# Kernel optimization log

Hardware: AMD Instinct MI355X
Metric: run time of the kernel (lower is better)

## Reference

```python
import jax, jax.numpy as jnp
import numpy as np

B, L, D = 32, 512, 128
H, D0, D2 = 8, 32, 32
SIGMA = 1.0
NEG = -10000.0


def setup_inputs() -> dict:
    key = jax.random.key(0)
    k_x, k_m, k1, k2, k3, k_w = jax.random.split(key, 6)
    X = jax.random.normal(k_x, (B, L, D), dtype=jnp.float32)
    # random padding mask; guarantee at least one valid item per row
    mask = jax.random.uniform(k_m, (B, L)) < 0.9
    mask = mask.at[:, 0].set(True)
    # nn.Linear(d, H*d0, bias=False): weight shape [H*d0, d], y = x @ W^T
    W1 = SIGMA * jax.random.normal(k1, (H * D0, D), dtype=jnp.float32)
    W2 = SIGMA * jax.random.normal(k2, (H * D0, D), dtype=jnp.float32)
    W3 = SIGMA * jax.random.normal(k3, (H * D2, D), dtype=jnp.float32)
    w = SIGMA * jax.random.normal(k_w, (H, D2), dtype=jnp.float32)
    return {"X": X, "mask": mask, "W1": W1, "W2": W2, "W3": W3, "w": w}


def reference(X, mask, W1, W2, W3, w):
    b, l, d = X.shape
    h, d2 = w.shape
    d0 = W1.shape[0] // h
    Q = (X @ W1.T).reshape(b, l, h, d0)
    K = (X @ W2.T).reshape(b, l, h, d0)
    V = (X @ W3.T).reshape(b, l, h, d2)
    # scores: [B, H, L, L]
    scores = jnp.einsum('blhd,bmhd->bhlm', Q, K) / jnp.sqrt(jnp.asarray(d0, X.dtype))
    # outer-product symmetric pad mask [B,1,L,L]
    am = (mask[:, None, None, :] & mask[:, None, :, None])
    scores = jnp.where(am, scores, jnp.asarray(NEG, X.dtype))
    attn = jax.nn.softmax(scores, axis=-1)
    out = jnp.einsum('bhlm,bmhd->blhd', attn, V)  # [B,L,H,D2]
    v = jnp.einsum('blhd,hd->bl', out, w) / jnp.sqrt(jnp.asarray(h, X.dtype))
    v = jnp.where(mask, v, jnp.asarray(NEG, X.dtype))
    probs = jax.nn.softmax(v, axis=-1)
    return probs
```

## Files before the change

kernel.cpp:

```cpp
#include <hip/hip_runtime.h>
#include <hip/hip_bf16.h>


typedef __attribute__((ext_vector_type(8))) short bf16x8;
typedef __attribute__((ext_vector_type(4))) float f32x4;
typedef __attribute__((ext_vector_type(8))) unsigned short ushort8;
typedef __attribute__((ext_vector_type(4))) unsigned short ushort4v;

#define NEG (-10000.0f)
#define LOG2E 1.4426950408889634f
#define QSCALE (0.17677669529663687f * LOG2E)

__device__ __forceinline__ unsigned short bf16_rn(float x, float* rep) {
  unsigned u = __float_as_uint(x);
  unsigned r = (u + 0x7FFFu + ((u >> 16) & 1u)) >> 16;
  *rep = __uint_as_float(r << 16);
  return (unsigned short)r;
}

__global__ __launch_bounds__(256) void convert_kernel(
    const float* __restrict__ X, const float* __restrict__ W1,
    const float* __restrict__ W2, const float* __restrict__ W3,
    const float* __restrict__ w,
    unsigned short* __restrict__ X2, unsigned short* __restrict__ Wc) {
  const int bx = blockIdx.x, t = threadIdx.x;
  if (bx < 1056) {
    const float* src;
    unsigned short* dst;
    int row, c;
    if (bx < 1024) {
      const size_t flat = (size_t)bx * 2048 + t * 8;
      row = (int)(flat >> 7); c = (int)(flat & 127);
      src = &X[flat];
      dst = &X2[(size_t)row * 256 + c];
    } else {
      const int flat = (bx - 1024) * 2048 + t * 8;
      row = flat >> 7; c = flat & 127;
      src = (row < 256) ? &W1[(size_t)row * 128 + c]
                        : &W2[(size_t)(row - 256) * 128 + c];
      dst = &Wc[(size_t)row * 256 + c];
    }
    float xv[8];
    *(float4*)&xv[0] = *(const float4*)src;
    *(float4*)&xv[4] = *(const float4*)(src + 4);
    ushort8 hi, lo;
#pragma unroll
    for (int i = 0; i < 8; ++i) {
      float hf, lf;
      hi[i] = bf16_rn(xv[i], &hf);
      lo[i] = bf16_rn(xv[i] - hf, &lf);
    }
    *(ushort8*)dst = hi;
    *(ushort8*)(dst + 128) = lo;
  } else {
    __shared__ float uS[8][128];
    if (t < 128) {
#pragma unroll
      for (int h = 0; h < 8; ++h) {
        float acc = 0.f;
#pragma unroll
        for (int d = 0; d < 32; ++d)
          acc += W3[(h * 32 + d) * 128 + t] * w[h * 32 + d];
        uS[h][t] = acc * 0.3535533905932738f;
      }
    }
    __syncthreads();
    {
      const int r = t >> 5, c = (t & 31) * 4;
      float4 v = *(float4*)&uS[r][c];
      float vv[4] = {v.x, v.y, v.z, v.w};
      ushort4v hi, lo;
#pragma unroll
      for (int i = 0; i < 4; ++i) {
        float hf, lf;
        hi[i] = bf16_rn(vv[i], &hf);
        lo[i] = bf16_rn(vv[i] - hf, &lf);
      }
      *(ushort4v*)&Wc[(size_t)(512 + r) * 256 + c] = hi;
      *(ushort4v*)&Wc[(size_t)(512 + r) * 256 + 128 + c] = lo;
    }
    const ushort8 z = {};
    for (int i = t; i < 1792; i += 256)
      *(ushort8*)&Wc[(size_t)520 * 256 + i * 8] = z;
  }
}

__global__ __launch_bounds__(256) void proj_kernel(
    const unsigned short* __restrict__ X2, const unsigned short* __restrict__ Wc,
    unsigned short* __restrict__ Q2, unsigned short* __restrict__ K2,
    float* __restrict__ Vw) {
  __shared__ unsigned short XS[128][72], WSd[64][72], WSx[64][72];
  const int t = threadIdx.x;
  const int row0 = blockIdx.x * 128, col0 = blockIdx.y * 64;
  const int w = t >> 6, lane = t & 63, g = lane >> 4, r16 = lane & 15;

  f32x4 acc[2][4];
#pragma unroll
  for (int mm = 0; mm < 2; ++mm)
#pragma unroll
    for (int n = 0; n < 4; ++n) acc[mm][n] = (f32x4){0.f, 0.f, 0.f, 0.f};

  for (int kc = 0; kc < 256; kc += 64) {
    const int kcx = (kc + 128) & 255;
    if (kc) __syncthreads();
    {
#pragma unroll
      for (int i = 0; i < 4; ++i) {
        const int flat = i * 256 + t, row = flat >> 3, cg = (flat & 7) * 8;
        *(ushort8*)&XS[row][cg] =
            *(const ushort8*)&X2[(size_t)(row0 + row) * 256 + kc + cg];
      }
#pragma unroll
      for (int i = 0; i < 2; ++i) {
        const int flat = i * 256 + t, row = flat >> 3, cg = (flat & 7) * 8;
        const size_t wb = (size_t)(col0 + row) * 256;
        *(ushort8*)&WSd[row][cg] = *(const ushort8*)&Wc[wb + kc + cg];
        *(ushort8*)&WSx[row][cg] = *(const ushort8*)&Wc[wb + kcx + cg];
      }
    }
    __syncthreads();
#pragma unroll
    for (int ks = 0; ks < 2; ++ks) {
      bf16x8 ah[2];
#pragma unroll
      for (int mm = 0; mm < 2; ++mm)
        ah[mm] = *(const bf16x8*)&XS[w * 32 + mm * 16 + r16][ks * 32 + g * 8];
#pragma unroll
      for (int n = 0; n < 4; ++n) {
        bf16x8 bd = *(const bf16x8*)&WSd[n * 16 + r16][ks * 32 + g * 8];
        bf16x8 bx = *(const bf16x8*)&WSx[n * 16 + r16][ks * 32 + g * 8];
#pragma unroll
        for (int mm = 0; mm < 2; ++mm) {
          acc[mm][n] = __builtin_amdgcn_mfma_f32_16x16x32_bf16(ah[mm], bd, acc[mm][n], 0, 0, 0);
          acc[mm][n] = __builtin_amdgcn_mfma_f32_16x16x32_bf16(ah[mm], bx, acc[mm][n], 0, 0, 0);
        }
      }
    }
  }
#pragma unroll
  for (int n = 0; n < 4; ++n) {
    const int col = col0 + n * 16 + r16;
#pragma unroll
    for (int mm = 0; mm < 2; ++mm) {
#pragma unroll
      for (int r = 0; r < 4; ++r) {
        const int row = row0 + w * 32 + mm * 16 + g * 4 + r;
        const int b = row >> 9, l = row & 511;
        const float val = acc[mm][n][r];
        if (col < 256) {
          const float sv = val * QSCALE;
          float hf, lf;
          const unsigned short hb = bf16_rn(sv, &hf);
          const unsigned short lb = bf16_rn(sv - hf, &lf);
          const size_t o = ((size_t)(b * 8 + (col >> 5)) * 512 + l) * 64 + (col & 31);
          Q2[o] = hb; Q2[o + 32] = lb;
        } else if (col < 512) {
          const int c2 = col - 256;
          float hf, lf;
          const unsigned short hb = bf16_rn(val, &hf);
          const unsigned short lb = bf16_rn(val - hf, &lf);
          const size_t o = ((size_t)(b * 8 + (c2 >> 5)) * 512 + l) * 64 + (c2 & 31);
          K2[o] = hb; K2[o + 32] = lb;
        } else if (col < 520) {
          Vw[(size_t)(b * 8 + (col - 512)) * 512 + l] = val;
        }
      }
    }
  }
}

__global__ __launch_bounds__(512, 4) void attn_kernel(
    const unsigned short* __restrict__ Q2, const unsigned short* __restrict__ K2,
    const float* __restrict__ Vw, const int* __restrict__ mask,
    float* __restrict__ vws) {
  __shared__ unsigned short KS[512][72];
  __shared__ float VwS[512], biasS[512];
  const int t = threadIdx.x;
  const int w = t >> 6, lane = t & 63, g = lane >> 4, r16 = lane & 15;
  const int qbase = blockIdx.x * 256, h = blockIdx.y, b = blockIdx.z;
  const size_t headoff = (size_t)(b * 8 + h) * 512;

#pragma unroll
  for (int i = 0; i < 8; ++i) {
    const int flat = i * 512 + t;
    const int row = flat >> 3, cg = (flat & 7) * 8;
    *(ushort8*)&KS[row][cg] = *(const ushort8*)&K2[(headoff + row) * 64 + cg];
  }
  VwS[t] = Vw[headoff + t];
  biasS[t] = mask[b * 512 + t] ? 0.f : NEG * LOG2E;

  bf16x8 qf[2][2];
#pragma unroll
  for (int qt = 0; qt < 2; ++qt)
#pragma unroll
    for (int ks = 0; ks < 2; ++ks)
      qf[qt][ks] = *(const bf16x8*)
          &Q2[(headoff + qbase + w * 32 + qt * 16 + r16) * 64 + ks * 32 + g * 8];

  __syncthreads();

  float m[2] = {-1e30f, -1e30f}, lsum[2] = {0.f, 0.f}, val[2] = {0.f, 0.f};

  for (int c = 0; c < 8; ++c) {
    bf16x8 a0[4], a1[4];
#pragma unroll
    for (int j = 0; j < 4; ++j) {
      a0[j] = *(const bf16x8*)&KS[c * 64 + j * 16 + r16][g * 8];
      a1[j] = *(const bf16x8*)&KS[c * 64 + j * 16 + r16][32 + g * 8];
    }
    f32x4 sc[4][2];
#pragma unroll
    for (int j = 0; j < 4; ++j)
#pragma unroll
      for (int qt = 0; qt < 2; ++qt) {
        f32x4 z = (f32x4){0.f, 0.f, 0.f, 0.f};
        z = __builtin_amdgcn_mfma_f32_16x16x32_bf16(a0[j], qf[qt][0], z, 0, 0, 0);
        z = __builtin_amdgcn_mfma_f32_16x16x32_bf16(a0[j], qf[qt][1], z, 0, 0, 0);
        z = __builtin_amdgcn_mfma_f32_16x16x32_bf16(a1[j], qf[qt][0], z, 0, 0, 0);
        sc[j][qt] = z;
      }
#pragma unroll
    for (int qt = 0; qt < 2; ++qt) {
      float sb[4][4];
      float cmax = -1e30f;
#pragma unroll
      for (int j = 0; j < 4; ++j) {
        const float4 bsj = *(const float4*)&biasS[c * 64 + j * 16 + g * 4];
        sb[j][0] = sc[j][qt][0] + bsj.x;
        sb[j][1] = sc[j][qt][1] + bsj.y;
        sb[j][2] = sc[j][qt][2] + bsj.z;
        sb[j][3] = sc[j][qt][3] + bsj.w;
#pragma unroll
        for (int r = 0; r < 4; ++r) cmax = fmaxf(cmax, sb[j][r]);
      }
      cmax = fmaxf(cmax, __shfl_xor(cmax, 16));
      cmax = fmaxf(cmax, __shfl_xor(cmax, 32));
      const float mnew = fmaxf(m[qt], cmax);
      const float f = __builtin_amdgcn_exp2f(m[qt] - mnew);
      m[qt] = mnew;
      float ls = lsum[qt] * f, vv = val[qt] * f;
#pragma unroll
      for (int j = 0; j < 4; ++j) {
        const float4 vwj = *(const float4*)&VwS[c * 64 + j * 16 + g * 4];
        const float p0 = __builtin_amdgcn_exp2f(sb[j][0] - mnew);
        const float p1 = __builtin_amdgcn_exp2f(sb[j][1] - mnew);
        const float p2 = __builtin_amdgcn_exp2f(sb[j][2] - mnew);
        const float p3 = __builtin_amdgcn_exp2f(sb[j][3] - mnew);
        ls += (p0 + p1) + (p2 + p3);
        vv = fmaf(p0, vwj.x, vv);
        vv = fmaf(p1, vwj.y, vv);
        vv = fmaf(p2, vwj.z, vv);
        vv = fmaf(p3, vwj.w, vv);
      }
      lsum[qt] = ls; val[qt] = vv;
    }
  }
#pragma unroll
  for (int qt = 0; qt < 2; ++qt) {
    lsum[qt] += __shfl_xor(lsum[qt], 16);
    val[qt]  += __shfl_xor(val[qt], 16);
    lsum[qt] += __shfl_xor(lsum[qt], 32);
    val[qt]  += __shfl_xor(val[qt], 32);
  }
  if (lane < 16) {
#pragma unroll
    for (int qt = 0; qt < 2; ++qt)
      vws[headoff + qbase + w * 32 + qt * 16 + lane] = val[qt] / lsum[qt];
  }
}

__global__ __launch_bounds__(512) void final_kernel(
    const float* __restrict__ vws, const int* __restrict__ mask,
    float* __restrict__ out) {
  const int b = blockIdx.x, l = threadIdx.x;
  __shared__ float redm[8], reds[8];
  float v = 0.f;
#pragma unroll
  for (int h = 0; h < 8; ++h) v += vws[(size_t)(b * 8 + h) * 512 + l];
  if (mask[b * 512 + l] == 0) v = NEG;
  float mx = v;
#pragma unroll
  for (int off = 32; off >= 1; off >>= 1) mx = fmaxf(mx, __shfl_xor(mx, off));
  if ((l & 63) == 0) redm[l >> 6] = mx;
  __syncthreads();
  float M = redm[0];
#pragma unroll
  for (int i = 1; i < 8; ++i) M = fmaxf(M, redm[i]);
  const float e = __expf(v - M);
  float sm = e;
#pragma unroll
  for (int off = 32; off >= 1; off >>= 1) sm += __shfl_xor(sm, off);
  if ((l & 63) == 0) reds[l >> 6] = sm;
  __syncthreads();
  float S = 0.f;
#pragma unroll
  for (int i = 0; i < 8; ++i) S += reds[i];
  out[b * 512 + l] = e / S;
}

extern "C" void kernel_launch(void* const* d_in, const int* in_sizes, int n_in,
                              void* d_out, int out_size, void* d_ws, size_t ws_size,
                              hipStream_t stream) {
  const float* X  = (const float*)d_in[0];
  const int*  mk  = (const int*)d_in[1];
  const float* W1 = (const float*)d_in[2];
  const float* W2 = (const float*)d_in[3];
  const float* W3 = (const float*)d_in[4];
  const float* w  = (const float*)d_in[5];
  float* out = (float*)d_out;

  char* ws = (char*)d_ws;
  unsigned short* X2 = (unsigned short*)ws;
  unsigned short* Wc = X2 + (size_t)16384 * 256;
  unsigned short* Q2 = Wc + (size_t)576 * 256;
  unsigned short* K2 = Q2 + (size_t)32 * 8 * 512 * 64;
  float* Vw  = (float*)(K2 + (size_t)32 * 8 * 512 * 64);
  float* vws = Vw + (size_t)32 * 8 * 512;

  convert_kernel<<<dim3(1057), dim3(256), 0, stream>>>(X, W1, W2, W3, w, X2, Wc);
  proj_kernel<<<dim3(128, 9), dim3(256), 0, stream>>>(X2, Wc, Q2, K2, Vw);
  attn_kernel<<<dim3(2, 8, 32), dim3(512), 0, stream>>>(Q2, K2, Vw, mk, vws);
  final_kernel<<<dim3(32), dim3(512), 0, stream>>>(vws, mk, out);
}
```

Before: 62.24 us.

## Fuse projection, attention and final softmax into a persistent kernel with grid barriers

Replaces the X conversion, projection, attention and final-softmax launches with one persistent 256-block kernel. X is split to bf16 hi/lo in shared memory, and software grid barriers separate the projection, attention and reduction phases. The X2 round-trip through global memory and several launch gaps are removed, and each attention block now covers a whole head (64 queries per wave). The cost is spin-wait barriers that rely on all 256 blocks being co-resident, fewer blocks in the attention phase, and a large shared-memory footprint per block.

```diff
diff --git a/kernel.cpp b/kernel.cpp
--- a/kernel.cpp
+++ b/kernel.cpp
@@ -18,28 +18,16 @@
   return (unsigned short)r;
 }
 
-__global__ __launch_bounds__(256) void convert_kernel(
-    const float* __restrict__ X, const float* __restrict__ W1,
-    const float* __restrict__ W2, const float* __restrict__ W3,
-    const float* __restrict__ w,
-    unsigned short* __restrict__ X2, unsigned short* __restrict__ Wc) {
+__global__ __launch_bounds__(256) void convert_w_kernel(
+    const float* __restrict__ W1, const float* __restrict__ W2,
+    const float* __restrict__ W3, const float* __restrict__ w,
+    unsigned short* __restrict__ Wc, int* __restrict__ bar) {
   const int bx = blockIdx.x, t = threadIdx.x;
-  if (bx < 1056) {
-    const float* src;
-    unsigned short* dst;
-    int row, c;
-    if (bx < 1024) {
-      const size_t flat = (size_t)bx * 2048 + t * 8;
-      row = (int)(flat >> 7); c = (int)(flat & 127);
-      src = &X[flat];
-      dst = &X2[(size_t)row * 256 + c];
-    } else {
-      const int flat = (bx - 1024) * 2048 + t * 8;
-      row = flat >> 7; c = flat & 127;
-      src = (row < 256) ? &W1[(size_t)row * 128 + c]
-                        : &W2[(size_t)(row - 256) * 128 + c];
-      dst = &Wc[(size_t)row * 256 + c];
-    }
+  if (bx < 32) {
+    const int flat = bx * 2048 + t * 8;
+    const int row = flat >> 7, c = flat & 127;
+    const float* src = (row < 256) ? &W1[(size_t)row * 128 + c]
+                                   : &W2[(size_t)(row - 256) * 128 + c];
     float xv[8];
     *(float4*)&xv[0] = *(const float4*)src;
     *(float4*)&xv[4] = *(const float4*)(src + 4);
@@ -50,6 +38,7 @@
       hi[i] = bf16_rn(xv[i], &hf);
       lo[i] = bf16_rn(xv[i] - hf, &lf);
     }
+    unsigned short* dst = &Wc[(size_t)row * 256 + c];
     *(ushort8*)dst = hi;
     *(ushort8*)(dst + 128) = lo;
   } else {
@@ -82,220 +71,245 @@
     const ushort8 z = {};
     for (int i = t; i < 1792; i += 256)
       *(ushort8*)&Wc[(size_t)520 * 256 + i * 8] = z;
-  }
-}
-
-__global__ __launch_bounds__(256) void proj_kernel(
-    const unsigned short* __restrict__ X2, const unsigned short* __restrict__ Wc,
-    unsigned short* __restrict__ Q2, unsigned short* __restrict__ K2,
-    float* __restrict__ Vw) {
-  __shared__ unsigned short XS[128][72], WSd[64][72], WSx[64][72];
-  const int t = threadIdx.x;
-  const int row0 = blockIdx.x * 128, col0 = blockIdx.y * 64;
-  const int w = t >> 6, lane = t & 63, g = lane >> 4, r16 = lane & 15;
-
-  f32x4 acc[2][4];
-#pragma unroll
-  for (int mm = 0; mm < 2; ++mm)
-#pragma unroll
-    for (int n = 0; n < 4; ++n) acc[mm][n] = (f32x4){0.f, 0.f, 0.f, 0.f};
-
-  for (int kc = 0; kc < 256; kc += 64) {
-    const int kcx = (kc + 128) & 255;
-    if (kc) __syncthreads();
+    if (t == 0) atomicExch(bar, 0);
+  }
+}
+
+__device__ __forceinline__ void grid_barrier(int* bar, int target) {
+  __syncthreads();
+  if (threadIdx.x == 0) {
+    __threadfence();
+    atomicAdd(bar, 1);
+    int tries = 0;
+    while (atomicAdd(bar, 0) < target && ++tries < 10000000)
+      __builtin_amdgcn_s_sleep(2);
+    __threadfence();
+  }
+  __syncthreads();
+}
+
+__global__ __launch_bounds__(512, 2) void mega_kernel(
+    const float* __restrict__ X, const unsigned short* __restrict__ Wc,
+    const int* __restrict__ mask, unsigned short* __restrict__ Q2,
+    unsigned short* __restrict__ K2, float* __restrict__ Vw,
+    float* __restrict__ vws, float* __restrict__ out, int* __restrict__ bar) {
+  __shared__ __align__(16) char smem[118272];
+  const int bid = blockIdx.x, t = threadIdx.x;
+  const int wid = t >> 6, lane = t & 63, g = lane >> 4, r16 = lane & 15;
+
+  {
+    unsigned short (*XS)[264] = (unsigned short(*)[264])smem;
+    unsigned short (*WS)[264] = (unsigned short(*)[264])(smem + 67584);
+    const int row0 = (bid >> 1) * 128, colbase = (bid & 1) * 288;
     {
-#pragma unroll
-      for (int i = 0; i < 4; ++i) {
-        const int flat = i * 256 + t, row = flat >> 3, cg = (flat & 7) * 8;
-        *(ushort8*)&XS[row][cg] =
-            *(const ushort8*)&X2[(size_t)(row0 + row) * 256 + kc + cg];
-      }
-#pragma unroll
-      for (int i = 0; i < 2; ++i) {
-        const int flat = i * 256 + t, row = flat >> 3, cg = (flat & 7) * 8;
-        const size_t wb = (size_t)(col0 + row) * 256;
-        *(ushort8*)&WSd[row][cg] = *(const ushort8*)&Wc[wb + kc + cg];
-        *(ushort8*)&WSx[row][cg] = *(const ushort8*)&Wc[wb + kcx + cg];
-      }
-    }
-    __syncthreads();
-#pragma unroll
-    for (int ks = 0; ks < 2; ++ks) {
-      bf16x8 ah[2];
+      const int row = t >> 2, cs = (t & 3) * 32;
+      const float* xp = &X[(size_t)(row0 + row) * 128 + cs];
+      float xv[32];
+#pragma unroll
+      for (int i = 0; i < 8; ++i) *(float4*)&xv[i * 4] = ((const float4*)xp)[i];
+#pragma unroll
+      for (int seg = 0; seg < 4; ++seg) {
+        ushort8 hi, lo;
+#pragma unroll
+        for (int e = 0; e < 8; ++e) {
+          float hf, lf;
+          hi[e] = bf16_rn(xv[seg * 8 + e], &hf);
+          lo[e] = bf16_rn(xv[seg * 8 + e] - hf, &lf);
+        }
+        *(ushort8*)&XS[row][cs + seg * 8] = hi;
+        *(ushort8*)&XS[row][128 + cs + seg * 8] = lo;
+      }
+    }
+    __syncthreads();
+    const int rowG = wid >> 1, colG = wid & 1;
+    for (int cc = 0; cc < 3; ++cc) {
+      const int col0 = colbase + cc * 96;
+      if (cc) __syncthreads();
+#pragma unroll
+      for (int i = 0; i < 6; ++i) {
+        const int flat = i * 512 + t, wr = flat >> 5, cg = (flat & 31) * 8;
+        *(ushort8*)&WS[wr][cg] = *(const ushort8*)&Wc[(size_t)(col0 + wr) * 256 + cg];
+      }
+      __syncthreads();
+      f32x4 acc[2][3];
 #pragma unroll
       for (int mm = 0; mm < 2; ++mm)
-        ah[mm] = *(const bf16x8*)&XS[w * 32 + mm * 16 + r16][ks * 32 + g * 8];
-#pragma unroll
-      for (int n = 0; n < 4; ++n) {
-        bf16x8 bd = *(const bf16x8*)&WSd[n * 16 + r16][ks * 32 + g * 8];
-        bf16x8 bx = *(const bf16x8*)&WSx[n * 16 + r16][ks * 32 + g * 8];
+#pragma unroll
+        for (int n = 0; n < 3; ++n) acc[mm][n] = (f32x4){0.f, 0.f, 0.f, 0.f};
+#pragma unroll
+      for (int kc = 0; kc < 256; kc += 64) {
+        const int kcx = (kc + 128) & 255;
+#pragma unroll
+        for (int ks = 0; ks < 2; ++ks) {
+          const int ko = kc + ks * 32 + g * 8, kox = kcx + ks * 32 + g * 8;
+          bf16x8 a0 = *(const bf16x8*)&XS[rowG * 32 + r16][ko];
+          bf16x8 a1 = *(const bf16x8*)&XS[rowG * 32 + 16 + r16][ko];
+#pragma unroll
+          for (int n = 0; n < 3; ++n) {
+            bf16x8 bd = *(const bf16x8*)&WS[colG * 48 + n * 16 + r16][ko];
+            bf16x8 bx = *(const bf16x8*)&WS[colG * 48 + n * 16 + r16][kox];
+            acc[0][n] = __builtin_amdgcn_mfma_f32_16x16x32_bf16(a0, bd, acc[0][n], 0, 0, 0);
+            acc[0][n] = __builtin_amdgcn_mfma_f32_16x16x32_bf16(a0, bx, acc[0][n], 0, 0, 0);
+            acc[1][n] = __builtin_amdgcn_mfma_f32_16x16x32_bf16(a1, bd, acc[1][n], 0, 0, 0);
+            acc[1][n] = __builtin_amdgcn_mfma_f32_16x16x32_bf16(a1, bx, acc[1][n], 0, 0, 0);
+          }
+        }
+      }
+#pragma unroll
+      for (int n = 0; n < 3; ++n) {
+        const int col = col0 + colG * 48 + n * 16 + r16;
 #pragma unroll
         for (int mm = 0; mm < 2; ++mm) {
-          acc[mm][n] = __builtin_amdgcn_mfma_f32_16x16x32_bf16(ah[mm], bd, acc[mm][n], 0, 0, 0);
-          acc[mm][n] = __builtin_amdgcn_mfma_f32_16x16x32_bf16(ah[mm], bx, acc[mm][n], 0, 0, 0);
-        }
-      }
-    }
-  }
-#pragma unroll
-  for (int n = 0; n < 4; ++n) {
-    const int col = col0 + n * 16 + r16;
-#pragma unroll
-    for (int mm = 0; mm < 2; ++mm) {
-#pragma unroll
-      for (int r = 0; r < 4; ++r) {
-        const int row = row0 + w * 32 + mm * 16 + g * 4 + r;
-        const int b = row >> 9, l = row & 511;
-        const float val = acc[mm][n][r];
-        if (col < 256) {
-          const float sv = val * QSCALE;
-          float hf, lf;
-          const unsigned short hb = bf16_rn(sv, &hf);
-          const unsigned short lb = bf16_rn(sv - hf, &lf);
-          const size_t o = ((size_t)(b * 8 + (col >> 5)) * 512 + l) * 64 + (col & 31);
-          Q2[o] = hb; Q2[o + 32] = lb;
-        } else if (col < 512) {
-          const int c2 = col - 256;
-          float hf, lf;
-          const unsigned short hb = bf16_rn(val, &hf);
-          const unsigned short lb = bf16_rn(val - hf, &lf);
-          const size_t o = ((size_t)(b * 8 + (c2 >> 5)) * 512 + l) * 64 + (c2 & 31);
-          K2[o] = hb; K2[o + 32] = lb;
-        } else if (col < 520) {
-          Vw[(size_t)(b * 8 + (col - 512)) * 512 + l] = val;
-        }
-      }
-    }
-  }
-}
-
-__global__ __launch_bounds__(512, 4) void attn_kernel(
-    const unsigned short* __restrict__ Q2, const unsigned short* __restrict__ K2,
-    const float* __restrict__ Vw, const int* __restrict__ mask,
-    float* __restrict__ vws) {
-  __shared__ unsigned short KS[512][72];
-  __shared__ float VwS[512], biasS[512];
-  const int t = threadIdx.x;
-  const int w = t >> 6, lane = t & 63, g = lane >> 4, r16 = lane & 15;
-  const int qbase = blockIdx.x * 256, h = blockIdx.y, b = blockIdx.z;
-  const size_t headoff = (size_t)(b * 8 + h) * 512;
-
-#pragma unroll
-  for (int i = 0; i < 8; ++i) {
-    const int flat = i * 512 + t;
-    const int row = flat >> 3, cg = (flat & 7) * 8;
-    *(ushort8*)&KS[row][cg] = *(const ushort8*)&K2[(headoff + row) * 64 + cg];
-  }
-  VwS[t] = Vw[headoff + t];
-  biasS[t] = mask[b * 512 + t] ? 0.f : NEG * LOG2E;
-
-  bf16x8 qf[2][2];
-#pragma unroll
-  for (int qt = 0; qt < 2; ++qt)
-#pragma unroll
-    for (int ks = 0; ks < 2; ++ks)
-      qf[qt][ks] = *(const bf16x8*)
-          &Q2[(headoff + qbase + w * 32 + qt * 16 + r16) * 64 + ks * 32 + g * 8];
-
-  __syncthreads();
-
-  float m[2] = {-1e30f, -1e30f}, lsum[2] = {0.f, 0.f}, val[2] = {0.f, 0.f};
-
-  for (int c = 0; c < 8; ++c) {
-    bf16x8 a0[4], a1[4];
-#pragma unroll
-    for (int j = 0; j < 4; ++j) {
-      a0[j] = *(const bf16x8*)&KS[c * 64 + j * 16 + r16][g * 8];
-      a1[j] = *(const bf16x8*)&KS[c * 64 + j * 16 + r16][32 + g * 8];
-    }
-    f32x4 sc[4][2];
-#pragma unroll
-    for (int j = 0; j < 4; ++j)
-#pragma unroll
-      for (int qt = 0; qt < 2; ++qt) {
-        f32x4 z = (f32x4){0.f, 0.f, 0.f, 0.f};
-        z = __builtin_amdgcn_mfma_f32_16x16x32_bf16(a0[j], qf[qt][0], z, 0, 0, 0);
-        z = __builtin_amdgcn_mfma_f32_16x16x32_bf16(a0[j], qf[qt][1], z, 0, 0, 0);
-        z = __builtin_amdgcn_mfma_f32_16x16x32_bf16(a1[j], qf[qt][0], z, 0, 0, 0);
-        sc[j][qt] = z;
-      }
-#pragma unroll
-    for (int qt = 0; qt < 2; ++qt) {
-      float sb[4][4];
-      float cmax = -1e30f;
+#pragma unroll
+          for (int r = 0; r < 4; ++r) {
+            const int row = row0 + rowG * 32 + mm * 16 + g * 4 + r;
+            const int b = row >> 9, l = row & 511;
+            const float val = acc[mm][n][r];
+            if (col < 256) {
+              const float sv = val * QSCALE;
+              float hf, lf;
+              const unsigned short hb = bf16_rn(sv, &hf);
+              const unsigned short lb = bf16_rn(sv - hf, &lf);
+              const size_t o = ((size_t)(b * 8 + (col >> 5)) * 512 + l) * 64 + (col & 31);
+              Q2[o] = hb; Q2[o + 32] = lb;
+            } else if (col < 512) {
+              const int c2 = col - 256;
+              float hf, lf;
+              const unsigned short hb = bf16_rn(val, &hf);
+              const unsigned short lb = bf16_rn(val - hf, &lf);
+              const size_t o = ((size_t)(b * 8 + (c2 >> 5)) * 512 + l) * 64 + (c2 & 31);
+              K2[o] = hb; K2[o + 32] = lb;
+            } else if (col < 520) {
+              Vw[(size_t)(b * 8 + (col - 512)) * 512 + l] = val;
+            }
+          }
+        }
+      }
+    }
+  }
+  grid_barrier(bar, 256);
+
+  {
+    unsigned short (*KS)[72] = (unsigned short(*)[72])smem;
+    float* VwS = (float*)(smem + 73728);
+    float* biasS = VwS + 512;
+    const int b = bid >> 3, h = bid & 7;
+    const size_t headoff = (size_t)(b * 8 + h) * 512;
+#pragma unroll
+    for (int i = 0; i < 8; ++i) {
+      const int flat = i * 512 + t, row = flat >> 3, cg = (flat & 7) * 8;
+      *(ushort8*)&KS[row][cg] = *(const ushort8*)&K2[(headoff + row) * 64 + cg];
+    }
+    VwS[t] = Vw[headoff + t];
+    biasS[t] = mask[b * 512 + t] ? 0.f : NEG * LOG2E;
+
+    bf16x8 qf[4][2];
+#pragma unroll
+    for (int qt = 0; qt < 4; ++qt)
+#pragma unroll
+      for (int ks = 0; ks < 2; ++ks)
+        qf[qt][ks] = *(const bf16x8*)
+            &Q2[(headoff + wid * 64 + qt * 16 + r16) * 64 + ks * 32 + g * 8];
+    __syncthreads();
+
+    float m[4], lsum[4], val[4];
+#pragma unroll
+    for (int qt = 0; qt < 4; ++qt) { m[qt] = -1e30f; lsum[qt] = 0.f; val[qt] = 0.f; }
+
+    for (int c = 0; c < 8; ++c) {
+      bf16x8 a0[4], a1[4];
 #pragma unroll
       for (int j = 0; j < 4; ++j) {
-        const float4 bsj = *(const float4*)&biasS[c * 64 + j * 16 + g * 4];
-        sb[j][0] = sc[j][qt][0] + bsj.x;
-        sb[j][1] = sc[j][qt][1] + bsj.y;
-        sb[j][2] = sc[j][qt][2] + bsj.z;
-        sb[j][3] = sc[j][qt][3] + bsj.w;
-#pragma unroll
-        for (int r = 0; r < 4; ++r) cmax = fmaxf(cmax, sb[j][r]);
-      }
-      cmax = fmaxf(cmax, __shfl_xor(cmax, 16));
-      cmax = fmaxf(cmax, __shfl_xor(cmax, 32));
-      const float mnew = fmaxf(m[qt], cmax);
-      const float f = __builtin_amdgcn_exp2f(m[qt] - mnew);
-      m[qt] = mnew;
-      float ls = lsum[qt] * f, vv = val[qt] * f;
-#pragma unroll
-      for (int j = 0; j < 4; ++j) {
-        const float4 vwj = *(const float4*)&VwS[c * 64 + j * 16 + g * 4];
-        const float p0 = __builtin_amdgcn_exp2f(sb[j][0] - mnew);
-        const float p1 = __builtin_amdgcn_exp2f(sb[j][1] - mnew);
-        const float p2 = __builtin_amdgcn_exp2f(sb[j][2] - mnew);
-        const float p3 = __builtin_amdgcn_exp2f(sb[j][3] - mnew);
-        ls += (p0 + p1) + (p2 + p3);
-        vv = fmaf(p0, vwj.x, vv);
-        vv = fmaf(p1, vwj.y, vv);
-        vv = fmaf(p2, vwj.z, vv);
-        vv = fmaf(p3, vwj.w, vv);
-      }
-      lsum[qt] = ls; val[qt] = vv;
-    }
-  }
-#pragma unroll
-  for (int qt = 0; qt < 2; ++qt) {
-    lsum[qt] += __shfl_xor(lsum[qt], 16);
-    val[qt]  += __shfl_xor(val[qt], 16);
-    lsum[qt] += __shfl_xor(lsum[qt], 32);
-    val[qt]  += __shfl_xor(val[qt], 32);
-  }
-  if (lane < 16) {
-#pragma unroll
-    for (int qt = 0; qt < 2; ++qt)
-      vws[headoff + qbase + w * 32 + qt * 16 + lane] = val[qt] / lsum[qt];
-  }
-}
-
-__global__ __launch_bounds__(512) void final_kernel(
-    const float* __restrict__ vws, const int* __restrict__ mask,
-    float* __restrict__ out) {
-  const int b = blockIdx.x, l = threadIdx.x;
-  __shared__ float redm[8], reds[8];
-  float v = 0.f;
-#pragma unroll
-  for (int h = 0; h < 8; ++h) v += vws[(size_t)(b * 8 + h) * 512 + l];
-  if (mask[b * 512 + l] == 0) v = NEG;
-  float mx = v;
-#pragma unroll
-  for (int off = 32; off >= 1; off >>= 1) mx = fmaxf(mx, __shfl_xor(mx, off));
-  if ((l & 63) == 0) redm[l >> 6] = mx;
-  __syncthreads();
-  float M = redm[0];
-#pragma unroll
-  for (int i = 1; i < 8; ++i) M = fmaxf(M, redm[i]);
-  const float e = __expf(v - M);
-  float sm = e;
-#pragma unroll
-  for (int off = 32; off >= 1; off >>= 1) sm += __shfl_xor(sm, off);
-  if ((l & 63) == 0) reds[l >> 6] = sm;
-  __syncthreads();
-  float S = 0.f;
-#pragma unroll
-  for (int i = 0; i < 8; ++i) S += reds[i];
-  out[b * 512 + l] = e / S;
+        a0[j] = *(const bf16x8*)&KS[c * 64 + j * 16 + r16][g * 8];
+        a1[j] = *(const bf16x8*)&KS[c * 64 + j * 16 + r16][32 + g * 8];
+      }
+#pragma unroll
+      for (int qt = 0; qt < 4; ++qt) {
+        f32x4 sc[4];
+#pragma unroll
+        for (int j = 0; j < 4; ++j) {
+          f32x4 z = (f32x4){0.f, 0.f, 0.f, 0.f};
+          z = __builtin_amdgcn_mfma_f32_16x16x32_bf16(a0[j], qf[qt][0], z, 0, 0, 0);
+          z = __builtin_amdgcn_mfma_f32_16x16x32_bf16(a0[j], qf[qt][1], z, 0, 0, 0);
+          z = __builtin_amdgcn_mfma_f32_16x16x32_bf16(a1[j], qf[qt][0], z, 0, 0, 0);
+          sc[j] = z;
+        }
+        float sb[4][4];
+        float cmax = -1e30f;
+#pragma unroll
+        for (int j = 0; j < 4; ++j) {
+          const float4 bsj = *(const float4*)&biasS[c * 64 + j * 16 + g * 4];
+          sb[j][0] = sc[j][0] + bsj.x;
+          sb[j][1] = sc[j][1] + bsj.y;
+          sb[j][2] = sc[j][2] + bsj.z;
+          sb[j][3] = sc[j][3] + bsj.w;
+#pragma unroll
+          for (int r = 0; r < 4; ++r) cmax = fmaxf(cmax, sb[j][r]);
+        }
+        cmax = fmaxf(cmax, __shfl_xor(cmax, 16));
+        cmax = fmaxf(cmax, __shfl_xor(cmax, 32));
+        const float mnew = fmaxf(m[qt], cmax);
+        const float f = __builtin_amdgcn_exp2f(m[qt] - mnew);
+        m[qt] = mnew;
+        float ls = lsum[qt] * f, vv = val[qt] * f;
+#pragma unroll
+        for (int j = 0; j < 4; ++j) {
+          const float4 vwj = *(const float4*)&VwS[c * 64 + j * 16 + g * 4];
+          const float p0 = __builtin_amdgcn_exp2f(sb[j][0] - mnew);
+          const float p1 = __builtin_amdgcn_exp2f(sb[j][1] - mnew);
+          const float p2 = __builtin_amdgcn_exp2f(sb[j][2] - mnew);
+          const float p3 = __builtin_amdgcn_exp2f(sb[j][3] - mnew);
+          ls += (p0 + p1) + (p2 + p3);
+          vv = fmaf(p0, vwj.x, vv);
+          vv = fmaf(p1, vwj.y, vv);
+          vv = fmaf(p2, vwj.z, vv);
+          vv = fmaf(p3, vwj.w, vv);
+        }
+        lsum[qt] = ls; val[qt] = vv;
+      }
+    }
+#pragma unroll
+    for (int qt = 0; qt < 4; ++qt) {
+      lsum[qt] += __shfl_xor(lsum[qt], 16);
+      val[qt]  += __shfl_xor(val[qt], 16);
+      lsum[qt] += __shfl_xor(lsum[qt], 32);
+      val[qt]  += __shfl_xor(val[qt], 32);
+    }
+    if (lane < 16) {
+#pragma unroll
+      for (int qt = 0; qt < 4; ++qt)
+        vws[headoff + wid * 64 + qt * 16 + lane] = val[qt] / lsum[qt];
+    }
+  }
+  grid_barrier(bar, 512);
+
+  if (bid < 32) {
+    float* redm = (float*)smem;
+    float* reds = redm + 8;
+    const int b = bid, l = t;
+    float v = 0.f;
+#pragma unroll
+    for (int h = 0; h < 8; ++h) v += vws[(size_t)(b * 8 + h) * 512 + l];
+    if (mask[b * 512 + l] == 0) v = NEG;
+    float mx = v;
+#pragma unroll
+    for (int off = 32; off >= 1; off >>= 1) mx = fmaxf(mx, __shfl_xor(mx, off));
+    if ((l & 63) == 0) redm[l >> 6] = mx;
+    __syncthreads();
+    float M = redm[0];
+#pragma unroll
+    for (int i = 1; i < 8; ++i) M = fmaxf(M, redm[i]);
+    const float e = __expf(v - M);
+    float sm = e;
+#pragma unroll
+    for (int off = 32; off >= 1; off >>= 1) sm += __shfl_xor(sm, off);
+    if ((l & 63) == 0) reds[l >> 6] = sm;
+    __syncthreads();
+    float S = 0.f;
+#pragma unroll
+    for (int i = 0; i < 8; ++i) S += reds[i];
+    out[b * 512 + l] = e / S;
+  }
 }
 
 extern "C" void kernel_launch(void* const* d_in, const int* in_sizes, int n_in,
@@ -310,15 +324,14 @@
   float* out = (float*)d_out;
 
   char* ws = (char*)d_ws;
-  unsigned short* X2 = (unsigned short*)ws;
-  unsigned short* Wc = X2 + (size_t)16384 * 256;
+  unsigned short* Wc = (unsigned short*)ws;
   unsigned short* Q2 = Wc + (size_t)576 * 256;
   unsigned short* K2 = Q2 + (size_t)32 * 8 * 512 * 64;
   float* Vw  = (float*)(K2 + (size_t)32 * 8 * 512 * 64);
   float* vws = Vw + (size_t)32 * 8 * 512;
-
-  convert_kernel<<<dim3(1057), dim3(256), 0, stream>>>(X, W1, W2, W3, w, X2, Wc);
-  proj_kernel<<<dim3(128, 9), dim3(256), 0, stream>>>(X2, Wc, Q2, K2, Vw);
-  attn_kernel<<<dim3(2, 8, 32), dim3(512), 0, stream>>>(Q2, K2, Vw, mk, vws);
-  final_kernel<<<dim3(32), dim3(512), 0, stream>>>(vws, mk, out);
-}
+  int* bar   = (int*)(vws + (size_t)32 * 8 * 512);
+
+  convert_w_kernel<<<dim3(33), dim3(256), 0, stream>>>(W1, W2, W3, w, Wc, bar);
+  mega_kernel<<<dim3(256), dim3(512), 0, stream>>>(X, Wc, mk, Q2, K2, Vw, vws,
+                                                   out, bar);
+}
```

New measurement: 89.95 us. +44.5%, slower.
